# Performance work log

Hardware: AMD Instinct MI355X
Metric: run time of the kernel (lower is better)

The kernel has to match this reference:

```python
import jax, jax.numpy as jnp
import numpy as np

B, S, D = 2, 2048, 1024
H = 16
HD = D // H


def setup_inputs() -> dict:
    key = jax.random.key(0)
    ks = jax.random.split(key, 6)
    X = jax.random.normal(ks[0], (B, S, D), dtype=jnp.float32)
    # Linear weights stored [in, out] so y = x @ W (torch stores transposed).
    sc = 1.0 / np.sqrt(D)
    Wq = jax.random.normal(ks[1], (D, D), dtype=jnp.float32) * sc
    Wk = jax.random.normal(ks[2], (D, D), dtype=jnp.float32) * sc
    Wv = jax.random.normal(ks[3], (D, D), dtype=jnp.float32) * sc
    Wo = jax.random.normal(ks[4], (D, D), dtype=jnp.float32) * sc
    bo = jax.random.normal(ks[5], (D,), dtype=jnp.float32) * 0.01
    return {"X": X, "Wq": Wq, "Wk": Wk, "Wv": Wv, "Wo": Wo, "bo": bo}


def reference(X, Wq, Wk, Wv, Wo, bo):
    b, n, _ = X.shape
    # QKV projections (no bias, qkv_bias=False), reshape to [b, h, n, hd]
    q = (X @ Wq).reshape(b, n, H, HD).transpose(0, 2, 1, 3)
    k = (X @ Wk).reshape(b, n, H, HD).transpose(0, 2, 1, 3)
    v = (X @ Wv).reshape(b, n, H, HD).transpose(0, 2, 1, 3)
    # Unscaled scores (module's scale flag defaults to False)
    scores = jnp.einsum("bhqd,bhkd->bhqk", q, k)
    causal = jnp.triu(jnp.ones((n, n), dtype=bool), k=1)  # True above diagonal
    scores = jnp.where(causal, -jnp.inf, scores)
    attn = jax.nn.softmax(scores, axis=-1)
    # dropout p=0.0 -> identity
    ctx = jnp.einsum("bhqk,bhkd->bqhd", attn, v).reshape(b, n, H * HD)
    return ctx @ Wo + bo
```

## Files before the change

kernel.cpp:

```cpp
#include <hip/hip_runtime.h>
#include <stdint.h>


typedef __attribute__((ext_vector_type(8))) short short8;
typedef __attribute__((ext_vector_type(4))) float floatx4;

#define S_LEN 2048
#define D_DIM 1024
#define NH 16
#define HD 64
#define L2E 1.44269504088896340736f

__device__ __forceinline__ short f2bf(float f) {
    uint32_t u = __builtin_bit_cast(uint32_t, f);
    uint32_t r = u + 0x7fffu + ((u >> 16) & 1u);
    return (short)(r >> 16);
}
__device__ __forceinline__ uint32_t pack2(float a, float b) {
#if __has_builtin(__builtin_amdgcn_cvt_pk_bf16_f32)
    auto v = __builtin_amdgcn_cvt_pk_bf16_f32(a, b);
    uint32_t r; __builtin_memcpy(&r, &v, sizeof(r)); return r;
#else
    return (uint32_t)(uint16_t)f2bf(a) | ((uint32_t)(uint16_t)f2bf(b) << 16);
#endif
}
__device__ __forceinline__ void gll16(const void* g, void* l) {
    __builtin_amdgcn_global_load_lds(
        (const __attribute__((address_space(1))) void*)g,
        (__attribute__((address_space(3))) void*)l, 16, 0, 0);
}

__global__ __launch_bounds__(256) void castx_kernel(const float* __restrict__ X,
                                                    short* __restrict__ Xb) {
    int i = blockIdx.x * 256 + threadIdx.x;
    const float4 v = *(const float4*)(X + (size_t)i * 4);
    uint2 o;
    o.x = pack2(v.x, v.y);
    o.y = pack2(v.z, v.w);
    *(uint2*)(Xb + (size_t)i * 4) = o;
}

__global__ __launch_bounds__(256) void tcast4_kernel(const float* __restrict__ Wq,
                                                     const float* __restrict__ Wk,
                                                     const float* __restrict__ Wv,
                                                     const float* __restrict__ Wo,
                                                     short* __restrict__ WqkvT,
                                                     short* __restrict__ WoT) {
    const int z = blockIdx.z;
    const float* W = (z == 0) ? Wq : (z == 1) ? Wk : (z == 2) ? Wv : Wo;
    short* WT = (z < 3) ? (WqkvT + (size_t)z * 1024 * 1024) : WoT;
    __shared__ float tile[32][33];
    const int bx = blockIdx.x * 32;
    const int by = blockIdx.y * 32;
    const int tx = threadIdx.x, ty = threadIdx.y;
    for (int i = 0; i < 32; i += 8)
        tile[ty + i][tx] = W[(size_t)(bx + ty + i) * D_DIM + by + tx];
    __syncthreads();
    for (int i = 0; i < 32; i += 8)
        WT[(size_t)(by + ty + i) * D_DIM + bx + tx] = f2bf(tile[tx][ty + i]);
}

__device__ __forceinline__ void gemm_main8(const short* __restrict__ A,
                                           const short* __restrict__ BT,
                                           short* As, short* Bs,
                                           int m0, int n0, floatx4 (&acc)[4][2],
                                           int tid) {
    const int lane = tid & 63, ln = lane & 15, quad = lane >> 4;
    const int wave = tid >> 6;
    const int mw = (wave & 1) * 64, nw = (wave >> 1) * 32;
    for (int k0 = 0; k0 < D_DIM; k0 += 64) {
        __syncthreads();
        for (int t = 0; t < 2; t++) {
            const int c = t * 512 + tid;
            const int row = c >> 3, pos = c & 7, src = pos ^ (row & 7);
            gll16(A  + (size_t)(m0 + row) * D_DIM + k0 + src * 8, As + c * 8);
            gll16(BT + (size_t)(n0 + row) * D_DIM + k0 + src * 8, Bs + c * 8);
        }
        __syncthreads();
        for (int ks = 0; ks < 2; ks++) {
            short8 a[4], b[2];
            for (int i = 0; i < 4; i++) {
                const int row = mw + i * 16 + ln;
                a[i] = *(const short8*)(As + row * 64 + (((ks * 4 + quad) ^ (ln & 7)) * 8));
            }
            for (int j = 0; j < 2; j++) {
                const int row = nw + j * 16 + ln;
                b[j] = *(const short8*)(Bs + row * 64 + (((ks * 4 + quad) ^ (ln & 7)) * 8));
            }
            for (int i = 0; i < 4; i++)
                for (int j = 0; j < 2; j++)
                    acc[i][j] = __builtin_amdgcn_mfma_f32_16x16x32_bf16(a[i], b[j], acc[i][j], 0, 0, 0);
        }
    }
}

__global__ __launch_bounds__(512) void gemm_qkv_kernel(const short* __restrict__ Xb,
                                                       const short* __restrict__ WT,
                                                       short* __restrict__ Qb,
                                                       short* __restrict__ Kb,
                                                       short* __restrict__ Vtb) {
    __shared__ __align__(16) short As[128 * 64];
    __shared__ __align__(16) short Bs[128 * 64];
    const int m0 = blockIdx.x * 128, n0 = blockIdx.y * 128;
    floatx4 acc[4][2] = {};
    gemm_main8(Xb, WT, As, Bs, m0, n0, acc, threadIdx.x);

    const int tid = threadIdx.x, wave = tid >> 6, lane = tid & 63;
    const int ln = lane & 15, quad = lane >> 4;
    const int mw = (wave & 1) * 64, nw = (wave >> 1) * 32;
    const int nsel = n0 >> 10;
    const float qs = (nsel == 0) ? L2E : 1.f;
    short* outB = (nsel == 0) ? Qb : (nsel == 1 ? Kb : Vtb);
    for (int i = 0; i < 4; i++)
        for (int j = 0; j < 2; j++)
            for (int r = 0; r < 4; r++) {
                const int row = m0 + mw + i * 16 + quad * 4 + r;
                const int col = (n0 & 1023) + nw + j * 16 + ln;
                const int bb = row >> 11, s = row & (S_LEN - 1);
                const int h = col >> 6, hd = col & (HD - 1);
                const short v = f2bf(acc[i][j][r] * qs);
                if (nsel < 2)
                    outB[(((size_t)(bb * NH + h)) * S_LEN + s) * HD + hd] = v;
                else
                    outB[(((size_t)(bb * NH + h)) * HD + hd) * S_LEN + s] = v;
            }
}

__global__ __launch_bounds__(512) void gemm_out_kernel(const short* __restrict__ Cb,
                                                       const short* __restrict__ WoT,
                                                       float* __restrict__ out,
                                                       const float* __restrict__ bias) {
    __shared__ __align__(16) short As[128 * 64];
    __shared__ __align__(16) short Bs[64 * 64];
    const int m0 = blockIdx.x * 128, n0 = blockIdx.y * 64;
    const int tid = threadIdx.x, lane = tid & 63;
    const int ln = lane & 15, quad = lane >> 4;
    const int wave = tid >> 6;
    const int mw = (wave & 3) * 32, nw = (wave >> 2) * 32;

    floatx4 acc[2][2] = {};

    for (int k0 = 0; k0 < D_DIM; k0 += 64) {
        __syncthreads();
        for (int t = 0; t < 2; t++) {
            const int c = t * 512 + tid;
            const int row = c >> 3, pos = c & 7, src = pos ^ (row & 7);
            gll16(Cb + (size_t)(m0 + row) * D_DIM + k0 + src * 8, As + c * 8);
        }
        {
            const int c = tid;
            const int row = c >> 3, pos = c & 7, src = pos ^ (row & 7);
            gll16(WoT + (size_t)(n0 + row) * D_DIM + k0 + src * 8, Bs + c * 8);
        }
        __syncthreads();
        for (int ks = 0; ks < 2; ks++) {
            short8 a[2], b[2];
            for (int i = 0; i < 2; i++) {
                const int row = mw + i * 16 + ln;
                a[i] = *(const short8*)(As + row * 64 + (((ks * 4 + quad) ^ (ln & 7)) * 8));
            }
            for (int j = 0; j < 2; j++) {
                const int row = nw + j * 16 + ln;
                b[j] = *(const short8*)(Bs + row * 64 + (((ks * 4 + quad) ^ (ln & 7)) * 8));
            }
            for (int i = 0; i < 2; i++)
                for (int j = 0; j < 2; j++)
                    acc[i][j] = __builtin_amdgcn_mfma_f32_16x16x32_bf16(a[i], b[j], acc[i][j], 0, 0, 0);
        }
    }

    for (int i = 0; i < 2; i++)
        for (int j = 0; j < 2; j++)
            for (int r = 0; r < 4; r++) {
                const int row = m0 + mw + i * 16 + quad * 4 + r;
                const int col = n0 + nw + j * 16 + ln;
                out[(size_t)row * D_DIM + col] = acc[i][j][r] + bias[col];
            }
}

__global__ __launch_bounds__(512, 6) void attn_kernel(const short* __restrict__ Q,
                                                      const short* __restrict__ Kg,
                                                      const short* __restrict__ Vt,
                                                      short* __restrict__ ctx,
                                                      float* __restrict__ Opart,
                                                      float* __restrict__ Lpart) {
    __shared__ __align__(16) short Ks[2][64 * 64];
    __shared__ __align__(16) short Vs[2][64 * 64];
    __shared__ __align__(16) short Ps[8][640];

    const int tid = threadIdx.x, wave = tid >> 6, lane = tid & 63;
    const int ln = lane & 15, quad = lane >> 4;

    const int id = blockIdx.x;
    const int bh = (id & 7) + 8 * ((id >> 3) & 3);
    const int t = id >> 5;

    static const unsigned char TASK[24] = {
        0xF0, 0x02, 0xF1, 0x12, 0xE1, 0x22, 0x72, 0x80,
        0xE0, 0x32, 0xD0, 0xA0, 0xD1, 0x90, 0xC1, 0x91,
        0xC0, 0x81, 0xB0, 0x42, 0xB1, 0xA1, 0x62, 0x52};
    const int code = TASK[t];
    const int qt = code >> 4, mode = code & 3;
    const int n = qt + 1, h0 = n >> 1;
    const int kb = 2 * ((mode == 1) ? h0 : 0);
    const int ke = 2 * ((mode == 0) ? h0 : n);
    const int pidx   = (mode == 2) ? -1 : ((qt - 8) * 32 + bh) * 2 + mode;
    const int kmask0 = 2 * qt;
    const int q0 = qt * 128;
    const int bb = bh >> 4, h = bh & 15;
    short* Pw = Ps[wave];

    const short* qrow = Q + ((size_t)bh * S_LEN + q0 + wave * 16 + ln) * HD;
    const short8 qb0 = *(const short8*)(qrow + quad * 8);
    const short8 qb1 = *(const short8*)(qrow + 32 + quad * 8);
    const int q_abs = q0 + wave * 16 + ln;

    const int srow = tid >> 3, spos = tid & 7, ssrc = spos ^ (srow & 7);
    const size_t kbase = (size_t)bh * S_LEN * HD;
    const size_t vbase = (size_t)bh * HD * S_LEN;

    float l_part = 0.f;
    floatx4 o_acc[4] = {};

#define STAGE(buf, kt_)                                                          \
    {                                                                            \
        const int k0s = (kt_) * 64;                                              \
        gll16(Kg + kbase + (size_t)(k0s + srow) * HD + ssrc * 8,                 \
              &Ks[buf][tid * 8]);                                                \
        gll16(Vt + vbase + (size_t)srow * S_LEN + k0s + ssrc * 8,                \
              &Vs[buf][tid * 8]);                                                \
    }

    int cur = 0;
    STAGE(0, kb);
    for (int kt = kb; kt < ke; kt++) {
        if (kt + 1 < ke) {
            STAGE(cur ^ 1, kt + 1);
            asm volatile("s_waitcnt vmcnt(2)" ::: "memory");
        } else {
            asm volatile("s_waitcnt vmcnt(0)" ::: "memory");
        }
        __builtin_amdgcn_s_barrier();
        __builtin_amdgcn_sched_barrier(0);

        const short* Kc = Ks[cur];
        const short* Vc = Vs[cur];

        floatx4 sc4[4];
        __builtin_amdgcn_s_setprio(1);
        for (int nt = 0; nt < 4; nt++) {
            const int row = nt * 16 + ln;
            const short8 ak0 = *(const short8*)(Kc + row * 64 + ((quad ^ (ln & 7)) * 8));
            const short8 ak1 = *(const short8*)(Kc + row * 64 + (((4 + quad) ^ (ln & 7)) * 8));
            floatx4 z = {};
            z = __builtin_amdgcn_mfma_f32_16x16x32_bf16(ak0, qb0, z, 0, 0, 0);
            z = __builtin_amdgcn_mfma_f32_16x16x32_bf16(ak1, qb1, z, 0, 0, 0);
            sc4[nt] = z;
        }
        __builtin_amdgcn_s_setprio(0);

        if (kt >= kmask0) {
            const int k0 = kt * 64;
            for (int nt = 0; nt < 4; nt++)
                for (int r = 0; r < 4; r++)
                    if (k0 + nt * 16 + quad * 4 + r > q_abs) sc4[nt][r] = -1e30f;
        }

        float ls = 0.f;
        for (int nt = 0; nt < 4; nt++)
            for (int r = 0; r < 4; r++) {
                const float e = exp2f(sc4[nt][r]);
                sc4[nt][r] = e; ls += e;
            }
        l_part += ls;

        for (int p = 0; p < 2; p++) {
            uint2 u0, u1;
            u0.x = pack2(sc4[2 * p][0], sc4[2 * p][1]);
            u0.y = pack2(sc4[2 * p][2], sc4[2 * p][3]);
            u1.x = pack2(sc4[2 * p + 1][0], sc4[2 * p + 1][1]);
            u1.y = pack2(sc4[2 * p + 1][2], sc4[2 * p + 1][3]);
            *(uint2*)&Pw[ln * 40 + quad * 4]      = u0;
            *(uint2*)&Pw[ln * 40 + 16 + quad * 4] = u1;
            const short8 bp = *(const short8*)&Pw[ln * 40 + quad * 8];
            __builtin_amdgcn_s_setprio(1);
            for (int dt = 0; dt < 4; dt++) {
                const int row = dt * 16 + ln;
                const short8 av = *(const short8*)(Vc + row * 64 + (((p * 4 + quad) ^ (ln & 7)) * 8));
                o_acc[dt] = __builtin_amdgcn_mfma_f32_16x16x32_bf16(av, bp, o_acc[dt], 0, 0, 0);
            }
            __builtin_amdgcn_s_setprio(0);
        }

        __builtin_amdgcn_sched_barrier(0);
        __builtin_amdgcn_s_barrier();
        cur ^= 1;
    }
#undef STAGE

    float l_tot = l_part;
    l_tot += __shfl_xor(l_tot, 16, 64);
    l_tot += __shfl_xor(l_tot, 32, 64);

    if (pidx >= 0) {
        float* Ob = Opart + (size_t)pidx * 8192 + (wave * 16 + ln) * 64;
        for (int dt = 0; dt < 4; dt++)
            *(float4*)(Ob + dt * 16 + quad * 4) = *(float4*)&o_acc[dt];
        if (quad == 0) Lpart[(size_t)pidx * 128 + wave * 16 + ln] = l_tot;
    } else {
        const float rl = 1.f / l_tot;
        const int qr = lane >> 2, sg = lane & 3;
        for (int c = 0; c < 2; c++) {
            for (int dd = 0; dd < 2; dd++) {
                const int dt = c * 2 + dd;
                uint2 u;
                u.x = pack2(o_acc[dt][0] * rl, o_acc[dt][1] * rl);
                u.y = pack2(o_acc[dt][2] * rl, o_acc[dt][3] * rl);
                *(uint2*)&Pw[ln * 40 + dd * 16 + quad * 4] = u;
            }
            const short8 v = *(const short8*)&Pw[qr * 40 + sg * 8];
            const int s = q0 + wave * 16 + qr;
            *(short8*)(ctx + ((size_t)bb * S_LEN + s) * D_DIM + h * HD + sg * 8 + c * 32) = v;
        }
    }
}

__global__ __launch_bounds__(256) void combine_kernel(const float* __restrict__ Opart,
                                                      const float* __restrict__ Lpart,
                                                      short* __restrict__ ctx) {
    const int tile = blockIdx.x;
    const int qt = 8 + (tile >> 5), bh = tile & 31;
    const int bb = bh >> 4, h = bh & 15;
    const int p0 = ((qt - 8) * 32 + bh) * 2;
    const float* O0 = Opart + (size_t)p0 * 8192;
    const float* O1 = O0 + 8192;
    const float* l0 = Lpart + (size_t)p0 * 128;
    const float* l1 = l0 + 128;
    for (int e = threadIdx.x; e < 2048; e += 256) {
        const int q = e >> 4, seg = e & 15;
        const float rl = 1.f / (l0[q] + l1[q]);
        const float4 x0 = *(const float4*)(O0 + q * 64 + seg * 4);
        const float4 x1 = *(const float4*)(O1 + q * 64 + seg * 4);
        uint2 u;
        u.x = pack2((x0.x + x1.x) * rl, (x0.y + x1.y) * rl);
        u.y = pack2((x0.z + x1.z) * rl, (x0.w + x1.w) * rl);
        const int s = qt * 128 + q;
        *(uint2*)(ctx + ((size_t)bb * S_LEN + s) * D_DIM + h * HD + seg * 4) = u;
    }
}

extern "C" void kernel_launch(void* const* d_in, const int* in_sizes, int n_in,
                              void* d_out, int out_size, void* d_ws, size_t ws_size,
                              hipStream_t stream) {
    const float* X  = (const float*)d_in[0];
    const float* Wq = (const float*)d_in[1];
    const float* Wk = (const float*)d_in[2];
    const float* Wv = (const float*)d_in[3];
    const float* Wo = (const float*)d_in[4];
    const float* bo = (const float*)d_in[5];
    float* out = (float*)d_out;

    char* ws = (char*)d_ws;
    const size_t MB = 1024 * 1024;
    short* Xb     = (short*)(ws);
    short* WqkvT  = (short*)(ws + 8  * MB);
    short* Qb     = (short*)(ws + 16 * MB);
    short* Kb     = (short*)(ws + 24 * MB);
    short* Vtb    = (short*)(ws + 32 * MB);
    short* ctxb   = (short*)(ws + 40 * MB);
    short* WoT    = (short*)(ws + 48 * MB);
    float* Opart  = (float*)(ws);
    float* Lpart  = (float*)(ws + 50 * MB);

    castx_kernel<<<4096, 256, 0, stream>>>(X, Xb);
    dim3 tg(32, 32, 4), tb(32, 8);
    tcast4_kernel<<<tg, tb, 0, stream>>>(Wq, Wk, Wv, Wo, WqkvT, WoT);

    dim3 gq(32, 24);
    gemm_qkv_kernel<<<gq, 512, 0, stream>>>(Xb, WqkvT, Qb, Kb, Vtb);

    attn_kernel<<<768, 512, 0, stream>>>(Qb, Kb, Vtb, ctxb, Opart, Lpart);
    combine_kernel<<<256, 256, 0, stream>>>(Opart, Lpart, ctxb);

    dim3 go(32, 16);
    gemm_out_kernel<<<go, 512, 0, stream>>>(ctxb, WoT, out, bo);
}
```

Measured before the change: 190.8 us.

## Double-buffer GEMM K-loops with async LDS loads and reorder attention task schedule

Rewrites both the QKV and output-projection GEMMs to use double-buffered 32-wide K tiles. The next tile's global-to-LDS load is issued before computing on the current one, with explicit vmcnt waits, raw barriers and raised priority around the MFMAs. It also sets an occupancy hint and reorders the attention task table so the heaviest split tiles are dispatched first and the unsplit short tiles last. This trades more barriers per K step (half-size tiles) for overlap of memory latency with compute.

```diff
diff --git a/kernel.cpp b/kernel.cpp
--- a/kernel.cpp
+++ b/kernel.cpp
@@ -60,54 +60,61 @@
         WT[(size_t)(by + ty + i) * D_DIM + bx + tx] = f2bf(tile[tx][ty + i]);
 }
 
-__device__ __forceinline__ void gemm_main8(const short* __restrict__ A,
-                                           const short* __restrict__ BT,
-                                           short* As, short* Bs,
-                                           int m0, int n0, floatx4 (&acc)[4][2],
-                                           int tid) {
-    const int lane = tid & 63, ln = lane & 15, quad = lane >> 4;
-    const int wave = tid >> 6;
-    const int mw = (wave & 1) * 64, nw = (wave >> 1) * 32;
-    for (int k0 = 0; k0 < D_DIM; k0 += 64) {
-        __syncthreads();
-        for (int t = 0; t < 2; t++) {
-            const int c = t * 512 + tid;
-            const int row = c >> 3, pos = c & 7, src = pos ^ (row & 7);
-            gll16(A  + (size_t)(m0 + row) * D_DIM + k0 + src * 8, As + c * 8);
-            gll16(BT + (size_t)(n0 + row) * D_DIM + k0 + src * 8, Bs + c * 8);
-        }
-        __syncthreads();
-        for (int ks = 0; ks < 2; ks++) {
-            short8 a[4], b[2];
-            for (int i = 0; i < 4; i++) {
-                const int row = mw + i * 16 + ln;
-                a[i] = *(const short8*)(As + row * 64 + (((ks * 4 + quad) ^ (ln & 7)) * 8));
-            }
-            for (int j = 0; j < 2; j++) {
-                const int row = nw + j * 16 + ln;
-                b[j] = *(const short8*)(Bs + row * 64 + (((ks * 4 + quad) ^ (ln & 7)) * 8));
-            }
-            for (int i = 0; i < 4; i++)
-                for (int j = 0; j < 2; j++)
-                    acc[i][j] = __builtin_amdgcn_mfma_f32_16x16x32_bf16(a[i], b[j], acc[i][j], 0, 0, 0);
-        }
-    }
-}
-
-__global__ __launch_bounds__(512) void gemm_qkv_kernel(const short* __restrict__ Xb,
-                                                       const short* __restrict__ WT,
-                                                       short* __restrict__ Qb,
-                                                       short* __restrict__ Kb,
-                                                       short* __restrict__ Vtb) {
-    __shared__ __align__(16) short As[128 * 64];
-    __shared__ __align__(16) short Bs[128 * 64];
+__global__ __launch_bounds__(512, 6) void gemm_qkv_kernel(const short* __restrict__ Xb,
+                                                          const short* __restrict__ WT,
+                                                          short* __restrict__ Qb,
+                                                          short* __restrict__ Kb,
+                                                          short* __restrict__ Vtb) {
+    __shared__ __align__(16) short As[2][128 * 32];
+    __shared__ __align__(16) short Bs[2][128 * 32];
     const int m0 = blockIdx.x * 128, n0 = blockIdx.y * 128;
-    floatx4 acc[4][2] = {};
-    gemm_main8(Xb, WT, As, Bs, m0, n0, acc, threadIdx.x);
-
-    const int tid = threadIdx.x, wave = tid >> 6, lane = tid & 63;
+    const int tid = threadIdx.x, lane = tid & 63, wave = tid >> 6;
     const int ln = lane & 15, quad = lane >> 4;
     const int mw = (wave & 1) * 64, nw = (wave >> 1) * 32;
+    floatx4 acc[4][2] = {};
+
+    const int srow = tid >> 2, ssrc = (tid & 3) ^ (srow & 3);
+    const short* Ab = Xb + (size_t)(m0 + srow) * D_DIM + ssrc * 8;
+    const short* Bb = WT + (size_t)(n0 + srow) * D_DIM + ssrc * 8;
+
+#define QSTAGE(buf, kk)                                   \
+    {                                                     \
+        gll16(Ab + (kk) * 32, &As[buf][tid * 8]);         \
+        gll16(Bb + (kk) * 32, &Bs[buf][tid * 8]);         \
+    }
+
+    QSTAGE(0, 0);
+    int cur = 0;
+    for (int kk = 0; kk < 32; kk++) {
+        if (kk + 1 < 32) {
+            QSTAGE(cur ^ 1, kk + 1);
+            asm volatile("s_waitcnt vmcnt(2)" ::: "memory");
+        } else {
+            asm volatile("s_waitcnt vmcnt(0)" ::: "memory");
+        }
+        __builtin_amdgcn_s_barrier();
+        __builtin_amdgcn_sched_barrier(0);
+        short8 a[4], b[2];
+        for (int i = 0; i < 4; i++) {
+            const int row = mw + i * 16 + ln;
+            a[i] = *(const short8*)(&As[cur][row * 32 + ((quad ^ (row & 3)) * 8)]);
+        }
+        for (int j = 0; j < 2; j++) {
+            const int row = nw + j * 16 + ln;
+            b[j] = *(const short8*)(&Bs[cur][row * 32 + ((quad ^ (row & 3)) * 8)]);
+        }
+        __builtin_amdgcn_s_setprio(1);
+        for (int i = 0; i < 4; i++)
+            for (int j = 0; j < 2; j++)
+                acc[i][j] = __builtin_amdgcn_mfma_f32_16x16x32_bf16(a[i], b[j], acc[i][j], 0, 0, 0);
+        __builtin_amdgcn_s_setprio(0);
+        __builtin_amdgcn_sched_barrier(0);
+        __builtin_amdgcn_s_barrier();
+        __builtin_amdgcn_sched_barrier(0);
+        cur ^= 1;
+    }
+#undef QSTAGE
+
     const int nsel = n0 >> 10;
     const float qs = (nsel == 0) ? L2E : 1.f;
     short* outB = (nsel == 0) ? Qb : (nsel == 1 ? Kb : Vtb);
@@ -126,48 +133,65 @@
             }
 }
 
-__global__ __launch_bounds__(512) void gemm_out_kernel(const short* __restrict__ Cb,
-                                                       const short* __restrict__ WoT,
-                                                       float* __restrict__ out,
-                                                       const float* __restrict__ bias) {
-    __shared__ __align__(16) short As[128 * 64];
-    __shared__ __align__(16) short Bs[64 * 64];
+__global__ __launch_bounds__(512, 6) void gemm_out_kernel(const short* __restrict__ Cb,
+                                                          const short* __restrict__ WoT,
+                                                          float* __restrict__ out,
+                                                          const float* __restrict__ bias) {
+    __shared__ __align__(16) short As[2][128 * 32];
+    __shared__ __align__(16) short Bs[2][64 * 32];
     const int m0 = blockIdx.x * 128, n0 = blockIdx.y * 64;
     const int tid = threadIdx.x, lane = tid & 63;
     const int ln = lane & 15, quad = lane >> 4;
     const int wave = tid >> 6;
     const int mw = (wave & 3) * 32, nw = (wave >> 2) * 32;
+    const bool heavy = (tid < 256);
 
     floatx4 acc[2][2] = {};
 
-    for (int k0 = 0; k0 < D_DIM; k0 += 64) {
-        __syncthreads();
-        for (int t = 0; t < 2; t++) {
-            const int c = t * 512 + tid;
-            const int row = c >> 3, pos = c & 7, src = pos ^ (row & 7);
-            gll16(Cb + (size_t)(m0 + row) * D_DIM + k0 + src * 8, As + c * 8);
-        }
-        {
-            const int c = tid;
-            const int row = c >> 3, pos = c & 7, src = pos ^ (row & 7);
-            gll16(WoT + (size_t)(n0 + row) * D_DIM + k0 + src * 8, Bs + c * 8);
-        }
-        __syncthreads();
-        for (int ks = 0; ks < 2; ks++) {
-            short8 a[2], b[2];
-            for (int i = 0; i < 2; i++) {
-                const int row = mw + i * 16 + ln;
-                a[i] = *(const short8*)(As + row * 64 + (((ks * 4 + quad) ^ (ln & 7)) * 8));
-            }
-            for (int j = 0; j < 2; j++) {
-                const int row = nw + j * 16 + ln;
-                b[j] = *(const short8*)(Bs + row * 64 + (((ks * 4 + quad) ^ (ln & 7)) * 8));
-            }
-            for (int i = 0; i < 2; i++)
-                for (int j = 0; j < 2; j++)
-                    acc[i][j] = __builtin_amdgcn_mfma_f32_16x16x32_bf16(a[i], b[j], acc[i][j], 0, 0, 0);
-        }
-    }
+    const int srow = tid >> 2, ssrc = (tid & 3) ^ (srow & 3);
+    const int tb = tid & 255;
+    const int brow = tb >> 2, bsrc = (tb & 3) ^ (brow & 3);
+    const short* Ab = Cb + (size_t)(m0 + srow) * D_DIM + ssrc * 8;
+    const short* Bb = WoT + (size_t)(n0 + brow) * D_DIM + bsrc * 8;
+
+#define OSTAGE(buf, kk)                                                \
+    {                                                                  \
+        gll16(Ab + (kk) * 32, &As[buf][tid * 8]);                      \
+        if (heavy) gll16(Bb + (kk) * 32, &Bs[buf][tb * 8]);            \
+    }
+
+    OSTAGE(0, 0);
+    int cur = 0;
+    for (int kk = 0; kk < 32; kk++) {
+        if (kk + 1 < 32) {
+            OSTAGE(cur ^ 1, kk + 1);
+            if (heavy) asm volatile("s_waitcnt vmcnt(2)" ::: "memory");
+            else       asm volatile("s_waitcnt vmcnt(1)" ::: "memory");
+        } else {
+            asm volatile("s_waitcnt vmcnt(0)" ::: "memory");
+        }
+        __builtin_amdgcn_s_barrier();
+        __builtin_amdgcn_sched_barrier(0);
+        short8 a[2], b[2];
+        for (int i = 0; i < 2; i++) {
+            const int row = mw + i * 16 + ln;
+            a[i] = *(const short8*)(&As[cur][row * 32 + ((quad ^ (row & 3)) * 8)]);
+        }
+        for (int j = 0; j < 2; j++) {
+            const int row = nw + j * 16 + ln;
+            b[j] = *(const short8*)(&Bs[cur][row * 32 + ((quad ^ (row & 3)) * 8)]);
+        }
+        __builtin_amdgcn_s_setprio(1);
+        for (int i = 0; i < 2; i++)
+            for (int j = 0; j < 2; j++)
+                acc[i][j] = __builtin_amdgcn_mfma_f32_16x16x32_bf16(a[i], b[j], acc[i][j], 0, 0, 0);
+        __builtin_amdgcn_s_setprio(0);
+        __builtin_amdgcn_sched_barrier(0);
+        __builtin_amdgcn_s_barrier();
+        __builtin_amdgcn_sched_barrier(0);
+        cur ^= 1;
+    }
+#undef OSTAGE
 
     for (int i = 0; i < 2; i++)
         for (int j = 0; j < 2; j++)
@@ -196,9 +220,9 @@
     const int t = id >> 5;
 
     static const unsigned char TASK[24] = {
-        0xF0, 0x02, 0xF1, 0x12, 0xE1, 0x22, 0x72, 0x80,
-        0xE0, 0x32, 0xD0, 0xA0, 0xD1, 0x90, 0xC1, 0x91,
-        0xC0, 0x81, 0xB0, 0x42, 0xB1, 0xA1, 0x62, 0x52};
+        0xF0, 0xE1, 0xD0, 0xC1, 0xB0, 0xA1, 0x90, 0x81,
+        0xF1, 0xE0, 0xD1, 0xC0, 0xB1, 0xA0, 0x91, 0x80,
+        0x02, 0x12, 0x22, 0x32, 0x42, 0x52, 0x62, 0x72};
     const int code = TASK[t];
     const int qt = code >> 4, mode = code & 3;
     const int n = qt + 1, h0 = n >> 1;
@@ -294,6 +318,7 @@
 
         __builtin_amdgcn_sched_barrier(0);
         __builtin_amdgcn_s_barrier();
+        __builtin_amdgcn_sched_barrier(0);
         cur ^= 1;
     }
 #undef STAGE
```

New measurement: 184.2 us. -3.4%, faster.
